# Kernel tuning notes

Hardware: AMD Instinct MI355X
Metric: run time of the kernel (lower is better)

The kernel has to match this reference:

```python
import jax, jax.numpy as jnp
import numpy as np

N, E = 50000, 800000
IN_DIM, HID, OUT, HEADS = 128, 128, 64, 4
C1 = HID // HEADS  # 32 per-head channels in gat1
NEG_SLOPE = 0.2


def _gat_conv(x, src, dst, W, a_src, a_dst, b, heads, ch):
    """PyG GATConv (inference): gather -> edge attention -> segment softmax -> scatter."""
    n = x.shape[0]
    h = (x @ W).reshape(n, heads, ch)                      # [N,H,C]
    alpha_src = jnp.einsum('nhc,hc->nh', h, a_src)         # [N,H]
    alpha_dst = jnp.einsum('nhc,hc->nh', h, a_dst)         # [N,H]
    e = jax.nn.leaky_relu(alpha_src[src] + alpha_dst[dst], NEG_SLOPE)  # [E,H]
    m = jax.ops.segment_max(e, dst, num_segments=n)        # per-target max (stable softmax)
    e = jnp.exp(e - m[dst])
    denom = jax.ops.segment_sum(e, dst, num_segments=n)
    alpha = e / (denom[dst] + 1e-16)                       # [E,H]
    out = jax.ops.segment_sum(h[src] * alpha[:, :, None], dst, num_segments=n)  # [N,H,C]
    return out.reshape(n, heads * ch) + b


def setup_inputs() -> dict:
    key = jax.random.key(0)
    ks = jax.random.split(key, 16)
    x = jax.random.normal(ks[0], (N, IN_DIM), dtype=jnp.float32)
    edge_index = jax.random.randint(ks[1], (2, E), 0, N, dtype=jnp.int64)
    s = lambda fan_in: 1.0 / np.sqrt(fan_in)
    return {
        'x': x,
        'edge_index': edge_index,
        'W1': jax.random.normal(ks[2], (IN_DIM, HEADS * C1), jnp.float32) * s(IN_DIM),
        'a_src1': jax.random.normal(ks[3], (HEADS, C1), jnp.float32) * s(C1),
        'a_dst1': jax.random.normal(ks[4], (HEADS, C1), jnp.float32) * s(C1),
        'b1': jnp.zeros((HID,), jnp.float32),
        'W2': jax.random.normal(ks[5], (HID, OUT), jnp.float32) * s(HID),
        'a_src2': jax.random.normal(ks[6], (1, OUT), jnp.float32) * s(OUT),
        'a_dst2': jax.random.normal(ks[7], (1, OUT), jnp.float32) * s(OUT),
        'b2': jnp.zeros((OUT,), jnp.float32),
        'pw1': jax.random.normal(ks[8], (OUT, OUT), jnp.float32) * s(OUT),
        'pb1': jnp.zeros((OUT,), jnp.float32),
        'pw2': jax.random.normal(ks[9], (OUT, OUT), jnp.float32) * s(OUT),
        'pb2': jnp.zeros((OUT,), jnp.float32),
    }


def reference(x, edge_index, W1, a_src1, a_dst1, b1, W2, a_src2, a_dst2, b2, pw1, pb1, pw2, pb2):
    n = x.shape[0]
    # PyG GATConv add_self_loops=True
    loops = jnp.arange(n, dtype=edge_index.dtype)
    src = jnp.concatenate([edge_index[0], loops])
    dst = jnp.concatenate([edge_index[1], loops])
    h = jax.nn.elu(_gat_conv(x, src, dst, W1, a_src1, a_dst1, b1, HEADS, C1))
    h = jax.nn.elu(_gat_conv(h, src, dst, W2, a_src2, a_dst2, b2, 1, OUT))
    # origin_proj: Linear -> ReLU -> Linear
    h = jax.nn.relu(h @ pw1 + pb1)
    return h @ pw2 + pb2
```

## Files before the change

### kernel.cpp

```cpp
#include <hip/hip_runtime.h>
#include <math.h>

#define N_NODES 50000
#define N_EDGES 800000
#define ET (N_EDGES + N_NODES)
#define IN_DIM 128
#define HID 128
#define OUT_DIM 64
#define BW 64
#define NBUCK ((N_NODES + BW - 1) / BW)
#define NBLK 256
#define EPB 3328
#define NT64 ((N_NODES + 63) / 64)

typedef __attribute__((ext_vector_type(8))) short bf16x8;
typedef __attribute__((ext_vector_type(4))) float f32x4;

__device__ __forceinline__ float lrelu(float x){ return x >= 0.f ? x : 0.2f * x; }
__device__ __forceinline__ float eluf(float x){ return x > 0.f ? x : expm1f(x); }
__device__ __forceinline__ unsigned f2bf(float f){
    unsigned u = __float_as_uint(f);
    return (u + 0x7fffu + ((u >> 16) & 1u)) >> 16;
}
__device__ __forceinline__ float bflo(unsigned u){ return __uint_as_float(u << 16); }
__device__ __forceinline__ float bfhi(unsigned u){ return __uint_as_float(u & 0xffff0000u); }

__global__ __launch_bounds__(256) void k_count(const int* __restrict__ dst, int* __restrict__ C)
{
    __shared__ int cnt[NBUCK];
    const int tid = threadIdx.x, blk = blockIdx.x;
    for (int i = tid; i < NBUCK; i += 256) cnt[i] = 0;
    __syncthreads();
    #pragma unroll
    for (int j = 0; j < EPB / 256; j++) {
        const int e = blk * EPB + j * 256 + tid;
        if (e < ET) {
            const int d = (e < N_EDGES) ? dst[e] : (e - N_EDGES);
            atomicAdd(&cnt[d >> 6], 1);
        }
    }
    __syncthreads();
    for (int b = tid; b < NBUCK; b += 256) C[b * NBLK + blk] = cnt[b];
}

__global__ __launch_bounds__(256) void k_bsumA(const int* __restrict__ C, int* __restrict__ bsum2)
{
    __shared__ int red[4];
    int v = C[blockIdx.x * NBLK + threadIdx.x];
    #pragma unroll
    for (int off = 32; off > 0; off >>= 1) v += __shfl_down(v, off);
    if ((threadIdx.x & 63) == 0) red[threadIdx.x >> 6] = v;
    __syncthreads();
    if (threadIdx.x == 0) bsum2[blockIdx.x] = red[0] + red[1] + red[2] + red[3];
}

__global__ __launch_bounds__(1024) void k_bscanB(const int* __restrict__ bsum2, int* __restrict__ boff2)
{
    __shared__ int part[1024];
    const int t = threadIdx.x;
    int v = (t < NBUCK) ? bsum2[t] : 0;
    part[t] = v;
    __syncthreads();
    #pragma unroll
    for (int d = 1; d < 1024; d <<= 1) {
        int add = (t >= d) ? part[t - d] : 0;
        __syncthreads();
        part[t] += add;
        __syncthreads();
    }
    if (t < NBUCK) boff2[t] = part[t] - v;
    if (t == 0) boff2[NBUCK] = ET;
}

__global__ __launch_bounds__(256) void k_cscanC(const int* __restrict__ C,
                                                const int* __restrict__ boff2,
                                                int* __restrict__ Cs)
{
    __shared__ int part[256];
    const int t = threadIdx.x, b = blockIdx.x;
    int v = C[b * NBLK + t];
    part[t] = v;
    __syncthreads();
    #pragma unroll
    for (int d = 1; d < 256; d <<= 1) {
        int add = (t >= d) ? part[t - d] : 0;
        __syncthreads();
        part[t] += add;
        __syncthreads();
    }
    Cs[b * NBLK + t] = boff2[b] + part[t] - v;
}

__global__ __launch_bounds__(256, 2) void k_gemm1_part2(
    const float* __restrict__ x, const float* __restrict__ W1,
    const float* __restrict__ a_s, const float* __restrict__ a_d,
    unsigned* __restrict__ h1b, float* __restrict__ as1, float* __restrict__ ad1,
    const int* __restrict__ src, const int* __restrict__ dst,
    const int* __restrict__ Cs, uint2* __restrict__ part)
{
    __shared__ unsigned smem[128 * 68 + 64 * 68];
    const int tid = threadIdx.x;

    if (blockIdx.x < NT64) {
        unsigned* sWt = smem;
        unsigned* sxb = smem + 128 * 68;
        const int wave = tid >> 6;
        const int lane = tid & 63;
        const int ll   = lane & 15;
        const int quad = lane >> 4;
        const int n0 = blockIdx.x * 64;

        for (int idx = tid; idx < 8192; idx += 256) {
            const int n = idx & 127, kp = idx >> 7;
            const float w0 = W1[(2 * kp) * 128 + n];
            const float w1 = W1[(2 * kp + 1) * 128 + n];
            sWt[n * 68 + kp] = f2bf(w0) | (f2bf(w1) << 16);
        }
        for (int idx = tid; idx < 4096; idx += 256) {
            const int node = idx >> 6, kp = idx & 63;
            const int n = n0 + node;
            unsigned pk = 0;
            if (n < N_NODES) {
                const float x0 = x[n * 128 + 2 * kp];
                const float x1 = x[n * 128 + 2 * kp + 1];
                pk = f2bf(x0) | (f2bf(x1) << 16);
            }
            sxb[node * 68 + kp] = pk;
        }
        __syncthreads();

        f32x4 acc[8];
        #pragma unroll
        for (int t = 0; t < 8; t++) acc[t] = (f32x4){0.f, 0.f, 0.f, 0.f};

        #pragma unroll
        for (int kk = 0; kk < 4; kk++) {
            const int kpo = 16 * kk + 4 * quad;
            const bf16x8 a = *(const bf16x8*)&sxb[(16 * wave + ll) * 68 + kpo];
            #pragma unroll
            for (int t = 0; t < 8; t++) {
                const bf16x8 b = *(const bf16x8*)&sWt[(16 * t + ll) * 68 + kpo];
                acc[t] = __builtin_amdgcn_mfma_f32_16x16x32_bf16(a, b, acc[t], 0, 0, 0);
            }
        }

        float as_v[8], ad_v[8];
        #pragma unroll
        for (int t = 0; t < 8; t++) { as_v[t] = a_s[16 * t + ll]; ad_v[t] = a_d[16 * t + ll]; }
        unsigned short* h1u = (unsigned short*)h1b;
        #pragma unroll
        for (int r = 0; r < 4; r++) {
            const int n = n0 + 16 * wave + 4 * quad + r;
            float ps0 = acc[0][r] * as_v[0] + acc[1][r] * as_v[1];
            float ps1 = acc[2][r] * as_v[2] + acc[3][r] * as_v[3];
            float ps2 = acc[4][r] * as_v[4] + acc[5][r] * as_v[5];
            float ps3 = acc[6][r] * as_v[6] + acc[7][r] * as_v[7];
            float pd0 = acc[0][r] * ad_v[0] + acc[1][r] * ad_v[1];
            float pd1 = acc[2][r] * ad_v[2] + acc[3][r] * ad_v[3];
            float pd2 = acc[4][r] * ad_v[4] + acc[5][r] * ad_v[5];
            float pd3 = acc[6][r] * ad_v[6] + acc[7][r] * ad_v[7];
            #pragma unroll
            for (int off = 1; off < 16; off <<= 1) {
                ps0 += __shfl_xor(ps0, off); ps1 += __shfl_xor(ps1, off);
                ps2 += __shfl_xor(ps2, off); ps3 += __shfl_xor(ps3, off);
                pd0 += __shfl_xor(pd0, off); pd1 += __shfl_xor(pd1, off);
                pd2 += __shfl_xor(pd2, off); pd3 += __shfl_xor(pd3, off);
            }
            if (n < N_NODES) {
                #pragma unroll
                for (int t = 0; t < 8; t++)
                    h1u[n * 128 + 16 * t + ll] = (unsigned short)f2bf(acc[t][r]);
                if (ll == 0) {
                    as1[n * 4 + 0] = ps0; as1[n * 4 + 1] = ps1;
                    as1[n * 4 + 2] = ps2; as1[n * 4 + 3] = ps3;
                    ad1[n * 4 + 0] = pd0; ad1[n * 4 + 1] = pd1;
                    ad1[n * 4 + 2] = pd2; ad1[n * 4 + 3] = pd3;
                }
            }
        }
    } else {
        const int blk = blockIdx.x - NT64;
        int* base = (int*)smem;
        int* cnt  = (int*)smem + NBUCK;
        for (int b = tid; b < NBUCK; b += 256) { base[b] = Cs[b * NBLK + blk]; cnt[b] = 0; }
        __syncthreads();
        #pragma unroll
        for (int j = 0; j < EPB / 256; j++) {
            const int e = blk * EPB + j * 256 + tid;
            if (e < ET) {
                int s, d;
                if (e < N_EDGES) { s = src[e]; d = dst[e]; } else { s = d = e - N_EDGES; }
                const int b = d >> 6;
                const int r = atomicAdd(&cnt[b], 1);
                part[base[b] + r] = make_uint2((unsigned)d, (unsigned)s);
            }
        }
    }
}

__global__ __launch_bounds__(256) void k_scat2(const int* __restrict__ boff2,
                                               const uint2* __restrict__ part,
                                               const float* __restrict__ as1,
                                               const float* __restrict__ ad1,
                                               int* __restrict__ rowptr,
                                               int* __restrict__ csr_src,
                                               float4* __restrict__ w1e)
{
    __shared__ int cnt64[BW];
    __shared__ int nbase[BW];
    __shared__ float4 sad[BW];
    const int b = blockIdx.x, tid = threadIdx.x;
    const int n0 = b * BW;
    const int lo = boff2[b], hi = boff2[b + 1];
    if (tid < BW) {
        cnt64[tid] = 0;
        const int n = n0 + tid;
        sad[tid] = (n < N_NODES) ? ((const float4*)ad1)[n] : make_float4(0.f, 0.f, 0.f, 0.f);
    }
    __syncthreads();
    for (int i = lo + tid; i < hi; i += 256) {
        atomicAdd(&cnt64[part[i].x & (BW - 1)], 1);
    }
    __syncthreads();
    if (tid < BW) {
        int v = cnt64[tid];
        int incl = v;
        #pragma unroll
        for (int off = 1; off < 64; off <<= 1) {
            int t2 = __shfl_up(incl, off);
            if (tid >= off) incl += t2;
        }
        const int excl = incl - v;
        nbase[tid] = excl;
        const int n = n0 + tid;
        if (n < N_NODES) rowptr[n] = lo + excl;
        cnt64[tid] = 0;
    }
    if (b == 0 && tid == 0) rowptr[N_NODES] = ET;
    __syncthreads();
    for (int i = lo + tid; i < hi; i += 256) {
        const uint2 p = part[i];
        const int dn = (int)p.x & (BW - 1);
        const int s  = (int)p.y;
        const int r = atomicAdd(&cnt64[dn], 1);
        const int pos = lo + nbase[dn] + r;
        csr_src[pos] = s;
        const float4 av = ((const float4*)as1)[s];
        const float4 dv = sad[dn];
        float4 w;
        w.x = expf(lrelu(av.x + dv.x));
        w.y = expf(lrelu(av.y + dv.y));
        w.z = expf(lrelu(av.z + dv.z));
        w.w = expf(lrelu(av.w + dv.w));
        w1e[pos] = w;
    }
}

__global__ __launch_bounds__(256) void k_aggr1(
    const int* __restrict__ rowptr, const int* __restrict__ csr_src,
    const float* __restrict__ w1e,
    const uint4* __restrict__ h1u4, const float* __restrict__ b1,
    unsigned* __restrict__ hEb)
{
    const int d  = blockIdx.x * 16 + (threadIdx.x >> 4);
    const int c8 = threadIdx.x & 15;
    const int hd = c8 >> 2;
    const int r0 = rowptr[d], r1 = rowptr[d + 1];
    float den = 0.f;
    float acc[8];
    #pragma unroll
    for (int m = 0; m < 8; m++) acc[m] = 0.f;
    int i = r0;
    for (; i + 4 <= r1; i += 4) {
        const int s0 = csr_src[i],     s1 = csr_src[i + 1];
        const int s2 = csr_src[i + 2], s3 = csr_src[i + 3];
        const float w0 = w1e[(i    ) * 4 + hd];
        const float w1 = w1e[(i + 1) * 4 + hd];
        const float w2 = w1e[(i + 2) * 4 + hd];
        const float w3 = w1e[(i + 3) * 4 + hd];
        const uint4 u0 = h1u4[s0 * 16 + c8];
        const uint4 u1 = h1u4[s1 * 16 + c8];
        const uint4 u2 = h1u4[s2 * 16 + c8];
        const uint4 u3 = h1u4[s3 * 16 + c8];
        den += (w0 + w1) + (w2 + w3);
        acc[0] = fmaf(bflo(u0.x), w0, acc[0]); acc[1] = fmaf(bfhi(u0.x), w0, acc[1]);
        acc[2] = fmaf(bflo(u0.y), w0, acc[2]); acc[3] = fmaf(bfhi(u0.y), w0, acc[3]);
        acc[4] = fmaf(bflo(u0.z), w0, acc[4]); acc[5] = fmaf(bfhi(u0.z), w0, acc[5]);
        acc[6] = fmaf(bflo(u0.w), w0, acc[6]); acc[7] = fmaf(bfhi(u0.w), w0, acc[7]);
        acc[0] = fmaf(bflo(u1.x), w1, acc[0]); acc[1] = fmaf(bfhi(u1.x), w1, acc[1]);
        acc[2] = fmaf(bflo(u1.y), w1, acc[2]); acc[3] = fmaf(bfhi(u1.y), w1, acc[3]);
        acc[4] = fmaf(bflo(u1.z), w1, acc[4]); acc[5] = fmaf(bfhi(u1.z), w1, acc[5]);
        acc[6] = fmaf(bflo(u1.w), w1, acc[6]); acc[7] = fmaf(bfhi(u1.w), w1, acc[7]);
        acc[0] = fmaf(bflo(u2.x), w2, acc[0]); acc[1] = fmaf(bfhi(u2.x), w2, acc[1]);
        acc[2] = fmaf(bflo(u2.y), w2, acc[2]); acc[3] = fmaf(bfhi(u2.y), w2, acc[3]);
        acc[4] = fmaf(bflo(u2.z), w2, acc[4]); acc[5] = fmaf(bfhi(u2.z), w2, acc[5]);
        acc[6] = fmaf(bflo(u2.w), w2, acc[6]); acc[7] = fmaf(bfhi(u2.w), w2, acc[7]);
        acc[0] = fmaf(bflo(u3.x), w3, acc[0]); acc[1] = fmaf(bfhi(u3.x), w3, acc[1]);
        acc[2] = fmaf(bflo(u3.y), w3, acc[2]); acc[3] = fmaf(bfhi(u3.y), w3, acc[3]);
        acc[4] = fmaf(bflo(u3.z), w3, acc[4]); acc[5] = fmaf(bfhi(u3.z), w3, acc[5]);
        acc[6] = fmaf(bflo(u3.w), w3, acc[6]); acc[7] = fmaf(bfhi(u3.w), w3, acc[7]);
    }
    for (; i < r1; ++i) {
        const int s = csr_src[i];
        const float w = w1e[i * 4 + hd];
        const uint4 u = h1u4[s * 16 + c8];
        den += w;
        acc[0] = fmaf(bflo(u.x), w, acc[0]); acc[1] = fmaf(bfhi(u.x), w, acc[1]);
        acc[2] = fmaf(bflo(u.y), w, acc[2]); acc[3] = fmaf(bfhi(u.y), w, acc[3]);
        acc[4] = fmaf(bflo(u.z), w, acc[4]); acc[5] = fmaf(bfhi(u.z), w, acc[5]);
        acc[6] = fmaf(bflo(u.w), w, acc[6]); acc[7] = fmaf(bfhi(u.w), w, acc[7]);
    }
    const float inv = 1.f / (den + 1e-16f);
    const float4 bA = ((const float4*)b1)[2 * c8];
    const float4 bB = ((const float4*)b1)[2 * c8 + 1];
    const float v0 = eluf(acc[0] * inv + bA.x);
    const float v1 = eluf(acc[1] * inv + bA.y);
    const float v2 = eluf(acc[2] * inv + bA.z);
    const float v3 = eluf(acc[3] * inv + bA.w);
    const float v4 = eluf(acc[4] * inv + bB.x);
    const float v5 = eluf(acc[5] * inv + bB.y);
    const float v6 = eluf(acc[6] * inv + bB.z);
    const float v7 = eluf(acc[7] * inv + bB.w);
    uint4 o;
    o.x = f2bf(v0) | (f2bf(v1) << 16);
    o.y = f2bf(v2) | (f2bf(v3) << 16);
    o.z = f2bf(v4) | (f2bf(v5) << 16);
    o.w = f2bf(v6) | (f2bf(v7) << 16);
    ((uint4*)hEb)[d * 16 + c8] = o;
}

__global__ __launch_bounds__(256, 4) void k_layer2(
    const unsigned* __restrict__ hEb,
    const float* __restrict__ W2, const float* __restrict__ a_s2, const float* __restrict__ a_d2,
    unsigned* __restrict__ h2b, float* __restrict__ as2, float* __restrict__ ad2)
{
    __shared__ unsigned sWt[64 * 68];
    __shared__ unsigned sxb[64 * 68];
    const int tid = threadIdx.x;
    const int wave = tid >> 6;
    const int lane = tid & 63;
    const int ll   = lane & 15;
    const int quad = lane >> 4;
    const int n0 = blockIdx.x * 64;

    for (int idx = tid; idx < 4096; idx += 256) {
        const int n = idx & 63, kp = idx >> 6;
        const float w0 = W2[(2 * kp) * 64 + n];
        const float w1 = W2[(2 * kp + 1) * 64 + n];
        sWt[n * 68 + kp] = f2bf(w0) | (f2bf(w1) << 16);
    }
    const uint4* hE4 = (const uint4*)hEb;
    for (int idx = tid; idx < 1024; idx += 256) {
        const int node = idx >> 4, q = idx & 15;
        const int n = n0 + node;
        uint4 pk = make_uint4(0, 0, 0, 0);
        if (n < N_NODES) pk = hE4[n * 16 + q];
        unsigned* dstp = &sxb[node * 68 + 4 * q];
        dstp[0] = pk.x; dstp[1] = pk.y; dstp[2] = pk.z; dstp[3] = pk.w;
    }
    __syncthreads();

    f32x4 acc[4];
    #pragma unroll
    for (int t = 0; t < 4; t++) acc[t] = (f32x4){0.f, 0.f, 0.f, 0.f};

    #pragma unroll
    for (int kk = 0; kk < 4; kk++) {
        const int kpo = 16 * kk + 4 * quad;
        const bf16x8 a = *(const bf16x8*)&sxb[(16 * wave + ll) * 68 + kpo];
        #pragma unroll
        for (int t = 0; t < 4; t++) {
            const bf16x8 b = *(const bf16x8*)&sWt[(16 * t + ll) * 68 + kpo];
            acc[t] = __builtin_amdgcn_mfma_f32_16x16x32_bf16(a, b, acc[t], 0, 0, 0);
        }
    }

    float as_v[4], ad_v[4];
    #pragma unroll
    for (int t = 0; t < 4; t++) { as_v[t] = a_s2[16 * t + ll]; ad_v[t] = a_d2[16 * t + ll]; }
    unsigned short* h2u = (unsigned short*)h2b;
    #pragma unroll
    for (int r = 0; r < 4; r++) {
        const int n = n0 + 16 * wave + 4 * quad + r;
        float ps = acc[0][r] * as_v[0] + acc[1][r] * as_v[1]
                 + acc[2][r] * as_v[2] + acc[3][r] * as_v[3];
        float pd = acc[0][r] * ad_v[0] + acc[1][r] * ad_v[1]
                 + acc[2][r] * ad_v[2] + acc[3][r] * ad_v[3];
        #pragma unroll
        for (int off = 1; off < 16; off <<= 1) {
            ps += __shfl_xor(ps, off);
            pd += __shfl_xor(pd, off);
        }
        if (n < N_NODES) {
            #pragma unroll
            for (int t = 0; t < 4; t++)
                h2u[n * 64 + 16 * t + ll] = (unsigned short)f2bf(acc[t][r]);
            if (ll == 0) { as2[n] = ps; ad2[n] = pd; }
        }
    }
}

__global__ __launch_bounds__(512, 4) void k_tail(
    const int* __restrict__ rowptr, const int* __restrict__ csr_src,
    const float* __restrict__ as2, const float* __restrict__ ad2,
    const uint4* __restrict__ h2u4, const float* __restrict__ b2,
    const float* __restrict__ pw1, const float* __restrict__ pb1,
    const float* __restrict__ pw2, const float* __restrict__ pb2,
    float* __restrict__ out)
{
    __shared__ float s1[64 * 64];
    __shared__ float s2[64 * 64];
    __shared__ float so[64][68];
    __shared__ float sp[64][68];
    const int tid = threadIdx.x;
    const int n0 = blockIdx.x * 64;

    for (int i = tid; i < 1024; i += 512) {
        ((float4*)s1)[i] = ((const float4*)pw1)[i];
        ((float4*)s2)[i] = ((const float4*)pw2)[i];
    }

    {
        const int dl = tid >> 3;
        const int c8 = tid & 7;
        const int d = n0 + dl;
        float acc[8];
        #pragma unroll
        for (int m = 0; m < 8; m++) acc[m] = 0.f;
        float v0 = 0.f, v1 = 0.f, v2 = 0.f, v3 = 0.f;
        float v4 = 0.f, v5 = 0.f, v6 = 0.f, v7 = 0.f;
        if (d < N_NODES) {
            const int r0 = rowptr[d], r1 = rowptr[d + 1];
            const float adv = ad2[d];
            float den = 0.f;
            int i = r0;
            for (; i + 4 <= r1; i += 4) {
                const int s0 = csr_src[i],      s1_ = csr_src[i + 1];
                const int s2_ = csr_src[i + 2], s3_ = csr_src[i + 3];
                const float e0 = as2[s0], e1 = as2[s1_], e2 = as2[s2_], e3 = as2[s3_];
                const uint4 u0 = h2u4[s0  * 8 + c8];
                const uint4 u1 = h2u4[s1_ * 8 + c8];
                const uint4 u2 = h2u4[s2_ * 8 + c8];
                const uint4 u3 = h2u4[s3_ * 8 + c8];
                const float w0 = expf(lrelu(e0 + adv));
                const float w1 = expf(lrelu(e1 + adv));
                const float w2 = expf(lrelu(e2 + adv));
                const float w3 = expf(lrelu(e3 + adv));
                den += (w0 + w1) + (w2 + w3);
                acc[0] = fmaf(bflo(u0.x), w0, acc[0]); acc[1] = fmaf(bfhi(u0.x), w0, acc[1]);
                acc[2] = fmaf(bflo(u0.y), w0, acc[2]); acc[3] = fmaf(bfhi(u0.y), w0, acc[3]);
                acc[4] = fmaf(bflo(u0.z), w0, acc[4]); acc[5] = fmaf(bfhi(u0.z), w0, acc[5]);
                acc[6] = fmaf(bflo(u0.w), w0, acc[6]); acc[7] = fmaf(bfhi(u0.w), w0, acc[7]);
                acc[0] = fmaf(bflo(u1.x), w1, acc[0]); acc[1] = fmaf(bfhi(u1.x), w1, acc[1]);
                acc[2] = fmaf(bflo(u1.y), w1, acc[2]); acc[3] = fmaf(bfhi(u1.y), w1, acc[3]);
                acc[4] = fmaf(bflo(u1.z), w1, acc[4]); acc[5] = fmaf(bfhi(u1.z), w1, acc[5]);
                acc[6] = fmaf(bflo(u1.w), w1, acc[6]); acc[7] = fmaf(bfhi(u1.w), w1, acc[7]);
                acc[0] = fmaf(bflo(u2.x), w2, acc[0]); acc[1] = fmaf(bfhi(u2.x), w2, acc[1]);
                acc[2] = fmaf(bflo(u2.y), w2, acc[2]); acc[3] = fmaf(bfhi(u2.y), w2, acc[3]);
                acc[4] = fmaf(bflo(u2.z), w2, acc[4]); acc[5] = fmaf(bfhi(u2.z), w2, acc[5]);
                acc[6] = fmaf(bflo(u2.w), w2, acc[6]); acc[7] = fmaf(bfhi(u2.w), w2, acc[7]);
                acc[0] = fmaf(bflo(u3.x), w3, acc[0]); acc[1] = fmaf(bfhi(u3.x), w3, acc[1]);
                acc[2] = fmaf(bflo(u3.y), w3, acc[2]); acc[3] = fmaf(bfhi(u3.y), w3, acc[3]);
                acc[4] = fmaf(bflo(u3.z), w3, acc[4]); acc[5] = fmaf(bfhi(u3.z), w3, acc[5]);
                acc[6] = fmaf(bflo(u3.w), w3, acc[6]); acc[7] = fmaf(bfhi(u3.w), w3, acc[7]);
            }
            for (; i < r1; ++i) {
                const int s = csr_src[i];
                const float w = expf(lrelu(as2[s] + adv));
                const uint4 u = h2u4[s * 8 + c8];
                den += w;
                acc[0] = fmaf(bflo(u.x), w, acc[0]); acc[1] = fmaf(bfhi(u.x), w, acc[1]);
                acc[2] = fmaf(bflo(u.y), w, acc[2]); acc[3] = fmaf(bfhi(u.y), w, acc[3]);
                acc[4] = fmaf(bflo(u.z), w, acc[4]); acc[5] = fmaf(bfhi(u.z), w, acc[5]);
                acc[6] = fmaf(bflo(u.w), w, acc[6]); acc[7] = fmaf(bfhi(u.w), w, acc[7]);
            }
            const float inv = 1.f / (den + 1e-16f);
            const float4 bA = ((const float4*)b2)[2 * c8];
            const float4 bB = ((const float4*)b2)[2 * c8 + 1];
            v0 = eluf(acc[0] * inv + bA.x);
            v1 = eluf(acc[1] * inv + bA.y);
            v2 = eluf(acc[2] * inv + bA.z);
            v3 = eluf(acc[3] * inv + bA.w);
            v4 = eluf(acc[4] * inv + bB.x);
            v5 = eluf(acc[5] * inv + bB.y);
            v6 = eluf(acc[6] * inv + bB.z);
            v7 = eluf(acc[7] * inv + bB.w);
        }
        *(float4*)&so[dl][8 * c8]     = make_float4(v0, v1, v2, v3);
        *(float4*)&so[dl][8 * c8 + 4] = make_float4(v4, v5, v6, v7);
    }
    __syncthreads();

    const int cg = tid & 15;
    const int ng = tid >> 4;
    const float4 pb1_4 = ((const float4*)pb1)[cg];
    const float4 pb2_4 = ((const float4*)pb2)[cg];
    float4 p[2];
    #pragma unroll
    for (int m = 0; m < 2; m++) p[m] = pb1_4;
    #pragma unroll 8
    for (int k = 0; k < 64; k++) {
        const float4 w = *(const float4*)&s1[k * 64 + 4 * cg];
        #pragma unroll
        for (int m = 0; m < 2; m++) {
            const float xv = so[2 * ng + m][k];
            p[m].x = fmaf(xv, w.x, p[m].x);
            p[m].y = fmaf(xv, w.y, p[m].y);
            p[m].z = fmaf(xv, w.z, p[m].z);
            p[m].w = fmaf(xv, w.w, p[m].w);
        }
    }
    #pragma unroll
    for (int m = 0; m < 2; m++) {
        p[m].x = fmaxf(p[m].x, 0.f); p[m].y = fmaxf(p[m].y, 0.f);
        p[m].z = fmaxf(p[m].z, 0.f); p[m].w = fmaxf(p[m].w, 0.f);
        *(float4*)&sp[2 * ng + m][4 * cg] = p[m];
    }
    __syncthreads();

    float4 o[2];
    #pragma unroll
    for (int m = 0; m < 2; m++) o[m] = pb2_4;
    #pragma unroll 8
    for (int k = 0; k < 64; k++) {
        const float4 w = *(const float4*)&s2[k * 64 + 4 * cg];
        #pragma unroll
        for (int m = 0; m < 2; m++) {
            const float xv = sp[2 * ng + m][k];
            o[m].x = fmaf(xv, w.x, o[m].x);
            o[m].y = fmaf(xv, w.y, o[m].y);
            o[m].z = fmaf(xv, w.z, o[m].z);
            o[m].w = fmaf(xv, w.w, o[m].w);
        }
    }
    #pragma unroll
    for (int m = 0; m < 2; m++) {
        const int n = n0 + 2 * ng + m;
        if (n < N_NODES) ((float4*)out)[n * 16 + cg] = o[m];
    }
}

extern "C" void kernel_launch(void* const* d_in, const int* in_sizes, int n_in,
                              void* d_out, int out_size, void* d_ws, size_t ws_size,
                              hipStream_t stream)
{
    const float* x      = (const float*)d_in[0];
    const int*   ei     = (const int*)d_in[1];
    const int*   src    = ei;
    const int*   dst    = ei + N_EDGES;
    const float* W1     = (const float*)d_in[2];
    const float* a_src1 = (const float*)d_in[3];
    const float* a_dst1 = (const float*)d_in[4];
    const float* b1     = (const float*)d_in[5];
    const float* W2     = (const float*)d_in[6];
    const float* a_src2 = (const float*)d_in[7];
    const float* a_dst2 = (const float*)d_in[8];
    const float* b2     = (const float*)d_in[9];
    const float* pw1    = (const float*)d_in[10];
    const float* pb1    = (const float*)d_in[11];
    const float* pw2    = (const float*)d_in[12];
    const float* pb2    = (const float*)d_in[13];

    uint2*  part = (uint2*)d_ws;
    float4* w1e  = (float4*)(part + ET);
    int* ibase   = (int*)(w1e + ET);
    int* rowptr  = ibase;
    int* C       = rowptr + 50001;
    int* Cs      = C + 200192;
    int* bsum2   = Cs + 200192;
    int* boff2   = bsum2 + 782;
    int* csr_src = boff2 + 785;
    unsigned* h1b = (unsigned*)(csr_src + 850000);
    unsigned* h2b = h1b + 3200000;
    float* fws   = (float*)(h2b + 1600000);
    float* as1   = fws;
    float* ad1   = as1 + 200000;
    unsigned* hEb = (unsigned*)(ad1 + 200000);
    float* as2   = (float*)(hEb + 3200000);
    float* ad2   = as2 + 50000;

    k_count<<<NBLK, 256, 0, stream>>>(dst, C);
    k_bsumA<<<NBUCK, 256, 0, stream>>>(C, bsum2);
    k_bscanB<<<1, 1024, 0, stream>>>(bsum2, boff2);
    k_cscanC<<<NBUCK, 256, 0, stream>>>(C, boff2, Cs);

    k_gemm1_part2<<<NT64 + NBLK, 256, 0, stream>>>(x, W1, a_src1, a_dst1,
                                                   h1b, as1, ad1,
                                                   src, dst, Cs, part);
    k_scat2<<<NBUCK, 256, 0, stream>>>(boff2, part, as1, ad1,
                                       rowptr, csr_src, w1e);

    k_aggr1<<<N_NODES / 16, 256, 0, stream>>>(rowptr, csr_src, (const float*)w1e,
                                              (const uint4*)h1b, b1, hEb);

    k_layer2<<<NT64, 256, 0, stream>>>(hEb, W2, a_src2, a_dst2, h2b, as2, ad2);

    k_tail<<<NT64, 512, 0, stream>>>(rowptr, csr_src, as2, ad2,
                                     (const uint4*)h2b, b2,
                                     pw1, pb1, pw2, pb2, (float*)d_out);
}
```

Before: 230.2 us.

## Increase partition blocks, pre-convert weights once, and split gemm1 from edge partitioning

Raises the edge-partition grid from 256 to 832 blocks with fewer edges per block, adjusting the count/scan kernels to handle the wider per-bucket column. W1 and W2 are converted to transposed bf16 once in an extra block of the count kernel, instead of being reconverted by every GEMM block. The fused gemm1+partition kernel is split into two separate launches. More blocks improve occupancy for the atomic partition pass but enlarge the count matrix and scans and add a launch, and splitting loses the overlap of GEMM and partition work.

```diff
diff --git a/kernel.cpp b/kernel.cpp
--- a/kernel.cpp
+++ b/kernel.cpp
@@ -9,8 +9,8 @@
 #define OUT_DIM 64
 #define BW 64
 #define NBUCK ((N_NODES + BW - 1) / BW)
-#define NBLK 256
-#define EPB 3328
+#define NBLK 832
+#define EPB 1024
 #define NT64 ((N_NODES + 63) / 64)
 
 typedef __attribute__((ext_vector_type(8))) short bf16x8;
@@ -25,10 +25,26 @@
 __device__ __forceinline__ float bflo(unsigned u){ return __uint_as_float(u << 16); }
 __device__ __forceinline__ float bfhi(unsigned u){ return __uint_as_float(u & 0xffff0000u); }
 
-__global__ __launch_bounds__(256) void k_count(const int* __restrict__ dst, int* __restrict__ C)
+__global__ __launch_bounds__(256) void k_count_prep(
+    const int* __restrict__ dst, int* __restrict__ C,
+    const float* __restrict__ W1, const float* __restrict__ W2,
+    unsigned* __restrict__ w1bT, unsigned* __restrict__ w2bT)
 {
     __shared__ int cnt[NBUCK];
     const int tid = threadIdx.x, blk = blockIdx.x;
+    if (blk == NBLK) {
+        for (int idx = tid; idx < 8192; idx += 256) {
+            const int n = idx & 127, kp = idx >> 7;
+            w1bT[n * 64 + kp] = f2bf(W1[(2 * kp) * 128 + n])
+                              | (f2bf(W1[(2 * kp + 1) * 128 + n]) << 16);
+        }
+        for (int idx = tid; idx < 4096; idx += 256) {
+            const int n = idx & 63, kp = idx >> 6;
+            w2bT[n * 64 + kp] = f2bf(W2[(2 * kp) * 64 + n])
+                              | (f2bf(W2[(2 * kp + 1) * 64 + n]) << 16);
+        }
+        return;
+    }
     for (int i = tid; i < NBUCK; i += 256) cnt[i] = 0;
     __syncthreads();
     #pragma unroll
@@ -46,7 +62,8 @@
 __global__ __launch_bounds__(256) void k_bsumA(const int* __restrict__ C, int* __restrict__ bsum2)
 {
     __shared__ int red[4];
-    int v = C[blockIdx.x * NBLK + threadIdx.x];
+    int v = 0;
+    for (int j = threadIdx.x; j < NBLK; j += 256) v += C[blockIdx.x * NBLK + j];
     #pragma unroll
     for (int off = 32; off > 0; off >>= 1) v += __shfl_down(v, off);
     if ((threadIdx.x & 63) == 0) red[threadIdx.x >> 6] = v;
@@ -72,128 +89,127 @@
     if (t == 0) boff2[NBUCK] = ET;
 }
 
-__global__ __launch_bounds__(256) void k_cscanC(const int* __restrict__ C,
-                                                const int* __restrict__ boff2,
-                                                int* __restrict__ Cs)
-{
-    __shared__ int part[256];
+__global__ __launch_bounds__(1024) void k_cscanC(const int* __restrict__ C,
+                                                 const int* __restrict__ boff2,
+                                                 int* __restrict__ Cs)
+{
+    __shared__ int part[1024];
     const int t = threadIdx.x, b = blockIdx.x;
-    int v = C[b * NBLK + t];
+    int v = (t < NBLK) ? C[b * NBLK + t] : 0;
     part[t] = v;
     __syncthreads();
     #pragma unroll
-    for (int d = 1; d < 256; d <<= 1) {
+    for (int d = 1; d < 1024; d <<= 1) {
         int add = (t >= d) ? part[t - d] : 0;
         __syncthreads();
         part[t] += add;
         __syncthreads();
     }
-    Cs[b * NBLK + t] = boff2[b] + part[t] - v;
-}
-
-__global__ __launch_bounds__(256, 2) void k_gemm1_part2(
-    const float* __restrict__ x, const float* __restrict__ W1,
+    if (t < NBLK) Cs[b * NBLK + t] = boff2[b] + part[t] - v;
+}
+
+__global__ __launch_bounds__(256, 2) void k_gemm1(
+    const float* __restrict__ x, const unsigned* __restrict__ w1bT,
     const float* __restrict__ a_s, const float* __restrict__ a_d,
-    unsigned* __restrict__ h1b, float* __restrict__ as1, float* __restrict__ ad1,
+    unsigned* __restrict__ h1b, float* __restrict__ as1, float* __restrict__ ad1)
+{
+    __shared__ unsigned sWt[128 * 68];
+    __shared__ unsigned sxb[64 * 68];
+    const int tid = threadIdx.x;
+    const int wave = tid >> 6;
+    const int lane = tid & 63;
+    const int ll   = lane & 15;
+    const int quad = lane >> 4;
+    const int n0 = blockIdx.x * 64;
+
+    for (int idx = tid; idx < 2048; idx += 256) {
+        const uint4 w = ((const uint4*)w1bT)[idx];
+        const int n = idx >> 4, q = idx & 15;
+        unsigned* dp = &sWt[n * 68 + 4 * q];
+        dp[0] = w.x; dp[1] = w.y; dp[2] = w.z; dp[3] = w.w;
+    }
+    for (int idx = tid; idx < 4096; idx += 256) {
+        const int node = idx >> 6, kp = idx & 63;
+        const int n = n0 + node;
+        unsigned pk = 0;
+        if (n < N_NODES) {
+            const float x0 = x[n * 128 + 2 * kp];
+            const float x1 = x[n * 128 + 2 * kp + 1];
+            pk = f2bf(x0) | (f2bf(x1) << 16);
+        }
+        sxb[node * 68 + kp] = pk;
+    }
+    __syncthreads();
+
+    f32x4 acc[8];
+    #pragma unroll
+    for (int t = 0; t < 8; t++) acc[t] = (f32x4){0.f, 0.f, 0.f, 0.f};
+
+    #pragma unroll
+    for (int kk = 0; kk < 4; kk++) {
+        const int kpo = 16 * kk + 4 * quad;
+        const bf16x8 a = *(const bf16x8*)&sxb[(16 * wave + ll) * 68 + kpo];
+        #pragma unroll
+        for (int t = 0; t < 8; t++) {
+            const bf16x8 b = *(const bf16x8*)&sWt[(16 * t + ll) * 68 + kpo];
+            acc[t] = __builtin_amdgcn_mfma_f32_16x16x32_bf16(a, b, acc[t], 0, 0, 0);
+        }
+    }
+
+    float as_v[8], ad_v[8];
+    #pragma unroll
+    for (int t = 0; t < 8; t++) { as_v[t] = a_s[16 * t + ll]; ad_v[t] = a_d[16 * t + ll]; }
+    unsigned short* h1u = (unsigned short*)h1b;
+    #pragma unroll
+    for (int r = 0; r < 4; r++) {
+        const int n = n0 + 16 * wave + 4 * quad + r;
+        float ps0 = acc[0][r] * as_v[0] + acc[1][r] * as_v[1];
+        float ps1 = acc[2][r] * as_v[2] + acc[3][r] * as_v[3];
+        float ps2 = acc[4][r] * as_v[4] + acc[5][r] * as_v[5];
+        float ps3 = acc[6][r] * as_v[6] + acc[7][r] * as_v[7];
+        float pd0 = acc[0][r] * ad_v[0] + acc[1][r] * ad_v[1];
+        float pd1 = acc[2][r] * ad_v[2] + acc[3][r] * ad_v[3];
+        float pd2 = acc[4][r] * ad_v[4] + acc[5][r] * ad_v[5];
+        float pd3 = acc[6][r] * ad_v[6] + acc[7][r] * ad_v[7];
+        #pragma unroll
+        for (int off = 1; off < 16; off <<= 1) {
+            ps0 += __shfl_xor(ps0, off); ps1 += __shfl_xor(ps1, off);
+            ps2 += __shfl_xor(ps2, off); ps3 += __shfl_xor(ps3, off);
+            pd0 += __shfl_xor(pd0, off); pd1 += __shfl_xor(pd1, off);
+            pd2 += __shfl_xor(pd2, off); pd3 += __shfl_xor(pd3, off);
+        }
+        if (n < N_NODES) {
+            #pragma unroll
+            for (int t = 0; t < 8; t++)
+                h1u[n * 128 + 16 * t + ll] = (unsigned short)f2bf(acc[t][r]);
+            if (ll == 0) {
+                as1[n * 4 + 0] = ps0; as1[n * 4 + 1] = ps1;
+                as1[n * 4 + 2] = ps2; as1[n * 4 + 3] = ps3;
+                ad1[n * 4 + 0] = pd0; ad1[n * 4 + 1] = pd1;
+                ad1[n * 4 + 2] = pd2; ad1[n * 4 + 3] = pd3;
+            }
+        }
+    }
+}
+
+__global__ __launch_bounds__(256) void k_part2(
     const int* __restrict__ src, const int* __restrict__ dst,
     const int* __restrict__ Cs, uint2* __restrict__ part)
 {
-    __shared__ unsigned smem[128 * 68 + 64 * 68];
-    const int tid = threadIdx.x;
-
-    if (blockIdx.x < NT64) {
-        unsigned* sWt = smem;
-        unsigned* sxb = smem + 128 * 68;
-        const int wave = tid >> 6;
-        const int lane = tid & 63;
-        const int ll   = lane & 15;
-        const int quad = lane >> 4;
-        const int n0 = blockIdx.x * 64;
-
-        for (int idx = tid; idx < 8192; idx += 256) {
-            const int n = idx & 127, kp = idx >> 7;
-            const float w0 = W1[(2 * kp) * 128 + n];
-            const float w1 = W1[(2 * kp + 1) * 128 + n];
-            sWt[n * 68 + kp] = f2bf(w0) | (f2bf(w1) << 16);
-        }
-        for (int idx = tid; idx < 4096; idx += 256) {
-            const int node = idx >> 6, kp = idx & 63;
-            const int n = n0 + node;
-            unsigned pk = 0;
-            if (n < N_NODES) {
-                const float x0 = x[n * 128 + 2 * kp];
-                const float x1 = x[n * 128 + 2 * kp + 1];
-                pk = f2bf(x0) | (f2bf(x1) << 16);
-            }
-            sxb[node * 68 + kp] = pk;
-        }
-        __syncthreads();
-
-        f32x4 acc[8];
-        #pragma unroll
-        for (int t = 0; t < 8; t++) acc[t] = (f32x4){0.f, 0.f, 0.f, 0.f};
-
-        #pragma unroll
-        for (int kk = 0; kk < 4; kk++) {
-            const int kpo = 16 * kk + 4 * quad;
-            const bf16x8 a = *(const bf16x8*)&sxb[(16 * wave + ll) * 68 + kpo];
-            #pragma unroll
-            for (int t = 0; t < 8; t++) {
-                const bf16x8 b = *(const bf16x8*)&sWt[(16 * t + ll) * 68 + kpo];
-                acc[t] = __builtin_amdgcn_mfma_f32_16x16x32_bf16(a, b, acc[t], 0, 0, 0);
-            }
-        }
-
-        float as_v[8], ad_v[8];
-        #pragma unroll
-        for (int t = 0; t < 8; t++) { as_v[t] = a_s[16 * t + ll]; ad_v[t] = a_d[16 * t + ll]; }
-        unsigned short* h1u = (unsigned short*)h1b;
-        #pragma unroll
-        for (int r = 0; r < 4; r++) {
-            const int n = n0 + 16 * wave + 4 * quad + r;
-            float ps0 = acc[0][r] * as_v[0] + acc[1][r] * as_v[1];
-            float ps1 = acc[2][r] * as_v[2] + acc[3][r] * as_v[3];
-            float ps2 = acc[4][r] * as_v[4] + acc[5][r] * as_v[5];
-            float ps3 = acc[6][r] * as_v[6] + acc[7][r] * as_v[7];
-            float pd0 = acc[0][r] * ad_v[0] + acc[1][r] * ad_v[1];
-            float pd1 = acc[2][r] * ad_v[2] + acc[3][r] * ad_v[3];
-            float pd2 = acc[4][r] * ad_v[4] + acc[5][r] * ad_v[5];
-            float pd3 = acc[6][r] * ad_v[6] + acc[7][r] * ad_v[7];
-            #pragma unroll
-            for (int off = 1; off < 16; off <<= 1) {
-                ps0 += __shfl_xor(ps0, off); ps1 += __shfl_xor(ps1, off);
-                ps2 += __shfl_xor(ps2, off); ps3 += __shfl_xor(ps3, off);
-                pd0 += __shfl_xor(pd0, off); pd1 += __shfl_xor(pd1, off);
-                pd2 += __shfl_xor(pd2, off); pd3 += __shfl_xor(pd3, off);
-            }
-            if (n < N_NODES) {
-                #pragma unroll
-                for (int t = 0; t < 8; t++)
-                    h1u[n * 128 + 16 * t + ll] = (unsigned short)f2bf(acc[t][r]);
-                if (ll == 0) {
-                    as1[n * 4 + 0] = ps0; as1[n * 4 + 1] = ps1;
-                    as1[n * 4 + 2] = ps2; as1[n * 4 + 3] = ps3;
-                    ad1[n * 4 + 0] = pd0; ad1[n * 4 + 1] = pd1;
-                    ad1[n * 4 + 2] = pd2; ad1[n * 4 + 3] = pd3;
-                }
-            }
-        }
-    } else {
-        const int blk = blockIdx.x - NT64;
-        int* base = (int*)smem;
-        int* cnt  = (int*)smem + NBUCK;
-        for (int b = tid; b < NBUCK; b += 256) { base[b] = Cs[b * NBLK + blk]; cnt[b] = 0; }
-        __syncthreads();
-        #pragma unroll
-        for (int j = 0; j < EPB / 256; j++) {
-            const int e = blk * EPB + j * 256 + tid;
-            if (e < ET) {
-                int s, d;
-                if (e < N_EDGES) { s = src[e]; d = dst[e]; } else { s = d = e - N_EDGES; }
-                const int b = d >> 6;
-                const int r = atomicAdd(&cnt[b], 1);
-                part[base[b] + r] = make_uint2((unsigned)d, (unsigned)s);
-            }
+    __shared__ int base[NBUCK];
+    __shared__ int cnt[NBUCK];
+    const int tid = threadIdx.x, blk = blockIdx.x;
+    for (int b = tid; b < NBUCK; b += 256) { base[b] = Cs[b * NBLK + blk]; cnt[b] = 0; }
+    __syncthreads();
+    #pragma unroll
+    for (int j = 0; j < EPB / 256; j++) {
+        const int e = blk * EPB + j * 256 + tid;
+        if (e < ET) {
+            int s, d;
+            if (e < N_EDGES) { s = src[e]; d = dst[e]; } else { s = d = e - N_EDGES; }
+            const int b = d >> 6;
+            const int r = atomicAdd(&cnt[b], 1);
+            part[base[b] + r] = make_uint2((unsigned)d, (unsigned)s);
         }
     }
 }
@@ -330,8 +346,8 @@
 }
 
 __global__ __launch_bounds__(256, 4) void k_layer2(
-    const unsigned* __restrict__ hEb,
-    const float* __restrict__ W2, const float* __restrict__ a_s2, const float* __restrict__ a_d2,
+    const unsigned* __restrict__ hEb, const unsigned* __restrict__ w2bT,
+    const float* __restrict__ a_s2, const float* __restrict__ a_d2,
     unsigned* __restrict__ h2b, float* __restrict__ as2, float* __restrict__ ad2)
 {
     __shared__ unsigned sWt[64 * 68];
@@ -343,11 +359,11 @@
     const int quad = lane >> 4;
     const int n0 = blockIdx.x * 64;
 
-    for (int idx = tid; idx < 4096; idx += 256) {
-        const int n = idx & 63, kp = idx >> 6;
-        const float w0 = W2[(2 * kp) * 64 + n];
-        const float w1 = W2[(2 * kp + 1) * 64 + n];
-        sWt[n * 68 + kp] = f2bf(w0) | (f2bf(w1) << 16);
+    for (int idx = tid; idx < 1024; idx += 256) {
+        const uint4 w = ((const uint4*)w2bT)[idx];
+        const int n = idx >> 4, q = idx & 15;
+        unsigned* dp = &sWt[n * 68 + 4 * q];
+        dp[0] = w.x; dp[1] = w.y; dp[2] = w.z; dp[3] = w.w;
     }
     const uint4* hE4 = (const uint4*)hEb;
     for (int idx = tid; idx < 1024; idx += 256) {
@@ -565,11 +581,11 @@
     float4* w1e  = (float4*)(part + ET);
     int* ibase   = (int*)(w1e + ET);
     int* rowptr  = ibase;
-    int* C       = rowptr + 50001;
-    int* Cs      = C + 200192;
-    int* bsum2   = Cs + 200192;
-    int* boff2   = bsum2 + 782;
-    int* csr_src = boff2 + 785;
+    int* C       = rowptr + 50004;
+    int* Cs      = C + 650624;
+    int* bsum2   = Cs + 650624;
+    int* boff2   = bsum2 + 784;
+    int* csr_src = boff2 + 784;
     unsigned* h1b = (unsigned*)(csr_src + 850000);
     unsigned* h2b = h1b + 3200000;
     float* fws   = (float*)(h2b + 1600000);
@@ -578,22 +594,25 @@
     unsigned* hEb = (unsigned*)(ad1 + 200000);
     float* as2   = (float*)(hEb + 3200000);
     float* ad2   = as2 + 50000;
-
-    k_count<<<NBLK, 256, 0, stream>>>(dst, C);
+    unsigned* w1bT = (unsigned*)(ad2 + 50000);
+    unsigned* w2bT = w1bT + 8192;
+
+    k_count_prep<<<NBLK + 1, 256, 0, stream>>>(dst, C, W1, W2, w1bT, w2bT);
     k_bsumA<<<NBUCK, 256, 0, stream>>>(C, bsum2);
     k_bscanB<<<1, 1024, 0, stream>>>(bsum2, boff2);
-    k_cscanC<<<NBUCK, 256, 0, stream>>>(C, boff2, Cs);
-
-    k_gemm1_part2<<<NT64 + NBLK, 256, 0, stream>>>(x, W1, a_src1, a_dst1,
-                                                   h1b, as1, ad1,
-                                                   src, dst, Cs, part);
+    k_cscanC<<<NBUCK, 1024, 0, stream>>>(C, boff2, Cs);
+
+    k_gemm1<<<NT64, 256, 0, stream>>>(x, w1bT, a_src1, a_dst1, h1b, as1, ad1);
+
+    k_part2<<<NBLK, 256, 0, stream>>>(src, dst, Cs, part);
+
     k_scat2<<<NBUCK, 256, 0, stream>>>(boff2, part, as1, ad1,
                                        rowptr, csr_src, w1e);
 
     k_aggr1<<<N_NODES / 16, 256, 0, stream>>>(rowptr, csr_src, (const float*)w1e,
                                               (const uint4*)h1b, b1, hEb);
 
-    k_layer2<<<NT64, 256, 0, stream>>>(hEb, W2, a_src2, a_dst2, h2b, as2, ad2);
+    k_layer2<<<NT64, 256, 0, stream>>>(hEb, w2bT, a_src2, a_dst2, h2b, as2, ad2);
 
     k_tail<<<NT64, 512, 0, stream>>>(rowptr, csr_src, as2, ad2,
                                      (const uint4*)h2b, b2,
```

New measurement: 265.2 us. 15.2% more time.
